# Kernel tuning notes

Measured on AMD Instinct MI355X. Metric: run time of the kernel, lower is better.

Reference implementation:

```python
import jax, jax.numpy as jnp
import numpy as np

N = 100000   # nodes
E = 1600000  # edges
F = 128      # in = hidden channels
L = 4        # num GCN layers
G = 512      # graphs in batch
OUT = 10     # classes
EPS = 1e-5


def setup_inputs() -> dict:
    key = jax.random.key(0)
    ks = jax.random.split(key, 12)
    x = jax.random.normal(ks[0], (N, F), dtype=jnp.float32)
    edge_index = jax.random.randint(ks[1], (2, E), 0, N, dtype=jnp.int64)
    batch = jnp.sort(jax.random.randint(ks[2], (N,), 0, G, dtype=jnp.int64))
    s = 1.0 / np.sqrt(F)
    Ws = jax.random.uniform(ks[3], (L, F, F), jnp.float32, -s, s)
    bs = jax.random.uniform(ks[4], (L, F), jnp.float32, -s, s)
    gammas = jnp.ones((L, F), jnp.float32)
    betas = jnp.zeros((L, F), jnp.float32)
    s1 = 1.0 / np.sqrt(F * L)
    W1 = jax.random.uniform(ks[5], (F * L, F), jnp.float32, -s1, s1)
    b1 = jax.random.uniform(ks[6], (F,), jnp.float32, -s1, s1)
    g1 = jnp.ones((F,), jnp.float32)
    bt1 = jnp.zeros((F,), jnp.float32)
    s2 = 1.0 / np.sqrt(F)
    W2 = jax.random.uniform(ks[7], (F, OUT), jnp.float32, -s2, s2)
    b2 = jax.random.uniform(ks[8], (OUT,), jnp.float32, -s2, s2)
    return {"x": x, "edge_index": edge_index, "batch": batch, "Ws": Ws, "bs": bs,
            "gammas": gammas, "betas": betas, "W1": W1, "b1": b1, "g1": g1,
            "bt1": bt1, "W2": W2, "b2": b2}


def _batch_norm(x, g, b):
    # training-mode BatchNorm1d over the node dim (biased variance)
    mu = jnp.mean(x, axis=0)
    var = jnp.var(x, axis=0)
    return (x - mu) * jax.lax.rsqrt(var + EPS) * g + b


def reference(x, edge_index, batch, Ws, bs, gammas, betas, W1, b1, g1, bt1, W2, b2):
    row, col = edge_index[0], edge_index[1]
    # GCN normalization (add_self_loops=False since normalize=True)
    deg = jax.ops.segment_sum(jnp.ones((E,), x.dtype), col, num_segments=N)
    dinv = jnp.where(deg > 0, jax.lax.rsqrt(deg), 0.0)
    norm = dinv[row] * dinv[col]  # [E]
    pooled = []
    h = x
    for t in range(L):
        hw = h @ Ws[t]                                    # [N, F]
        msg = norm[:, None] * hw[row]                     # gather  [E, F]
        h = jax.ops.segment_sum(msg, col, num_segments=N) + bs[t]  # scatter [N, F]
        h = jax.nn.relu(h)
        h = _batch_norm(h, gammas[t], betas[t])
        pooled.append(jax.ops.segment_sum(h, batch, num_segments=G))  # [G, F]
    z = jnp.concatenate(pooled, axis=1)                   # [G, L*F]
    z = z @ W1 + b1
    z = _batch_norm(z, g1, bt1)
    z = jax.nn.relu(z)
    return z @ W2 + b2                                    # [G, OUT]
```

## Files before the change

kernel.cpp:

```cpp
#include <hip/hip_runtime.h>

#define NN 100000
#define EE 1600000
#define FF 128
#define LL 4
#define GG 512
#define OUTC 10
#define EPSF 1e-5f
#define NSCB ((NN + 255) / 256)

typedef __attribute__((ext_vector_type(8))) short short8;
typedef __attribute__((ext_vector_type(4))) float f32x4;

__device__ inline unsigned bf16rne(float f) {
  unsigned u = __float_as_uint(f);
  return (u + 0x7fffu + ((u >> 16) & 1u)) >> 16;
}
__device__ inline unsigned packbf(float lo, float hi) {
  return bf16rne(lo) | (bf16rne(hi) << 16);
}
__device__ inline float bflo(unsigned u) { return __uint_as_float(u << 16); }
__device__ inline float bfhi(unsigned u) { return __uint_as_float(u & 0xffff0000u); }


__global__ __launch_bounds__(256) void k_deg(const int* __restrict__ col, int* __restrict__ deg) {
  int e = blockIdx.x * 256 + threadIdx.x;
  if (e < EE) atomicAdd(&deg[col[e]], 1);
}

__global__ __launch_bounds__(256) void k_dinv(const int* __restrict__ deg, float* __restrict__ dinv) {
  int n = blockIdx.x * 256 + threadIdx.x;
  if (n < NN) {
    int d = deg[n];
    dinv[n] = d > 0 ? rsqrtf((float)d) : 0.0f;
  }
}

__global__ __launch_bounds__(256) void k_bsum(const int* __restrict__ deg, int* __restrict__ bsum) {
  int i = blockIdx.x * 256 + threadIdx.x;
  int v = (i < NN) ? deg[i] : 0;
#pragma unroll
  for (int off = 32; off > 0; off >>= 1) v += __shfl_down(v, off, 64);
  __shared__ int ws[4];
  if ((threadIdx.x & 63) == 0) ws[threadIdx.x >> 6] = v;
  __syncthreads();
  if (threadIdx.x == 0) bsum[blockIdx.x] = ws[0] + ws[1] + ws[2] + ws[3];
}

__global__ __launch_bounds__(256) void k_rowptr(const int* __restrict__ deg,
                                                const int* __restrict__ bsum,
                                                int* __restrict__ rowptr) {
  __shared__ int sb[512];
  __shared__ int sd[256];
  const int t = threadIdx.x;
  sb[t]       = (t < NSCB) ? bsum[t] : 0;
  sb[t + 256] = (t + 256 < NSCB) ? bsum[t + 256] : 0;
  __syncthreads();
#pragma unroll
  for (int off = 1; off < 512; off <<= 1) {
    int v0 = (t >= off) ? sb[t - off] : 0;
    int v1 = sb[t + 256 - off];
    __syncthreads();
    sb[t] += v0;
    sb[t + 256] += v1;
    __syncthreads();
  }
  const int bpre = (blockIdx.x == 0) ? 0 : sb[blockIdx.x - 1];
  const int i = blockIdx.x * 256 + t;
  const int d = (i < NN) ? deg[i] : 0;
  sd[t] = d;
  __syncthreads();
#pragma unroll
  for (int off = 1; off < 256; off <<= 1) {
    int v = (t >= off) ? sd[t - off] : 0;
    __syncthreads();
    sd[t] += v;
    __syncthreads();
  }
  if (i < NN) rowptr[i] = bpre + sd[t] - d;
  if (blockIdx.x == 0 && t == 0) rowptr[NN] = EE;
}

__global__ __launch_bounds__(256) void k_fill(const int* __restrict__ ei,
                                              const int* __restrict__ rowptr,
                                              int* __restrict__ cnt,
                                              const float* __restrict__ dinv,
                                              int2* __restrict__ ecw) {
  int e = blockIdx.x * 256 + threadIdx.x;
  if (e >= EE) return;
  int r = ei[e];
  int cl = ei[EE + e];
  int slot = rowptr[cl] + atomicAdd(&cnt[cl], 1);
  ecw[slot] = make_int2(r, __float_as_int(dinv[r] * dinv[cl]));
}

__global__ __launch_bounds__(256) void k_bounds(const int* __restrict__ batch, int* __restrict__ gstart) {
  int n = blockIdx.x * 256 + threadIdx.x;
  if (n >= NN) return;
  int b = batch[n];
  if (n == 0) {
    for (int g = 0; g <= b; ++g) gstart[g] = 0;
  } else {
    int bp = batch[n - 1];
    for (int g = bp + 1; g <= b; ++g) gstart[g] = n;
  }
  if (n == NN - 1) {
    for (int g = b + 1; g <= GG; ++g) gstart[g] = NN;
  }
}


__global__ __launch_bounds__(256) void k_cvt(const float* __restrict__ x, unsigned* __restrict__ Ab) {
  int i = blockIdx.x * 256 + threadIdx.x;
  if (i < NN * 64) {
    float2 v = *(const float2*)(x + (size_t)i * 2);
    Ab[i] = packbf(v.x, v.y);
  }
}

__global__ __launch_bounds__(256) void k_wcvt(const float* __restrict__ Ws, uint4* __restrict__ Wf) {
  int tid = blockIdx.x * 256 + threadIdx.x;
  int t = tid >> 12;
  int r = tid & 4095;
  int lane = r & 63;
  int which = (r >> 6) & 1;
  int ct = (r >> 7) & 7;
  int kc = r >> 10;
  int n = ct * 16 + (lane & 15);
  int k0 = kc * 32 + (lane >> 4) * 8;
  const float* W = Ws + t * 16384;
  unsigned h[8];
#pragma unroll
  for (int j = 0; j < 8; ++j) {
    float w = W[(k0 + j) * 128 + n];
    unsigned hb = bf16rne(w);
    if (which == 0) {
      h[j] = hb;
    } else {
      float hf = __uint_as_float(hb << 16);
      h[j] = bf16rne(w - hf);
    }
  }
  uint4 o;
  o.x = h[0] | (h[1] << 16);
  o.y = h[2] | (h[3] << 16);
  o.z = h[4] | (h[5] << 16);
  o.w = h[6] | (h[7] << 16);
  Wf[tid] = o;
}

__global__ __launch_bounds__(256) void k_mm(const unsigned* __restrict__ Ab,
                                            const uint4* __restrict__ Wf,
                                            unsigned* __restrict__ Bb) {
  const int lane = threadIdx.x & 63;
  const int w = threadIdx.x >> 6;
  const int quad = lane >> 4;
  const int m = lane & 15;
  const int rowbase = blockIdx.x * 64 + w * 16;
  const int arow = min(rowbase + m, NN - 1);
  const uint4* A4 = (const uint4*)Ab;
  f32x4 acc[8];
#pragma unroll
  for (int ct = 0; ct < 8; ++ct) acc[ct] = (f32x4){0.f, 0.f, 0.f, 0.f};
#pragma unroll
  for (int kc = 0; kc < 4; ++kc) {
    uint4 av = A4[arow * 16 + kc * 4 + quad];
    short8 af = *(short8*)&av;
#pragma unroll
    for (int ct = 0; ct < 8; ++ct) {
      uint4 bh = Wf[((kc * 8 + ct) * 2 + 0) * 64 + lane];
      uint4 bl = Wf[((kc * 8 + ct) * 2 + 1) * 64 + lane];
      acc[ct] = __builtin_amdgcn_mfma_f32_16x16x32_bf16(af, *(short8*)&bh, acc[ct], 0, 0, 0);
      acc[ct] = __builtin_amdgcn_mfma_f32_16x16x32_bf16(af, *(short8*)&bl, acc[ct], 0, 0, 0);
    }
  }
#pragma unroll
  for (int ct = 0; ct < 8; ++ct) {
#pragma unroll
    for (int r = 0; r < 4; ++r) {
      float v = acc[ct][r];
      float vo = __shfl_xor(v, 1);
      int row = rowbase + quad * 4 + r;
      if ((lane & 1) == 0 && row < NN) {
        Bb[row * 64 + ct * 8 + (m >> 1)] = packbf(v, vo);
      }
    }
  }
}

__global__ __launch_bounds__(256) void k_agg(const unsigned* __restrict__ Bb,
                                             const int* __restrict__ rowptr,
                                             const int2* __restrict__ ecw,
                                             const float* __restrict__ bias,
                                             unsigned* __restrict__ Ar,
                                             float* __restrict__ bnbuf) {
  const int lane = threadIdx.x & 63;
  const int wave = threadIdx.x >> 6;
  const int c = lane * 2;
  const int gwave = blockIdx.x * 4 + wave;
  const int nwaves = gridDim.x * 4;
  const float2 bv = *(const float2*)(bias + c);
  float s0 = 0.f, s1 = 0.f, q0 = 0.f, q1 = 0.f;
  for (int n = gwave; n < NN; n += nwaves) {
    const int beg = rowptr[n];
    const int end = rowptr[n + 1];
    float ax[8], ay[8];
#pragma unroll
    for (int j = 0; j < 8; ++j) { ax[j] = 0.f; ay[j] = 0.f; }
    int2 stage = (beg + lane < end) ? ecw[beg + lane] : make_int2(0, 0);
    for (int base = beg; base < end; base += 64) {
      const int2 cur = stage;
      const int nb = base + 64;
      if (nb < end) {
        const int j = nb + lane;
        stage = (j < end) ? ecw[j] : make_int2(0, 0);
      }
#pragma unroll
      for (int g = 0; g < 4; ++g) {
        if (base + g * 16 < end) {
          int is[16]; float wv[16]; unsigned us[16];
#pragma unroll
          for (int j = 0; j < 16; ++j) {
            is[j] = __shfl(cur.x, g * 16 + j);
            wv[j] = __shfl(__int_as_float(cur.y), g * 16 + j);
          }
#pragma unroll
          for (int j = 0; j < 16; ++j) us[j] = Bb[((unsigned)is[j] << 6) + (unsigned)lane];
#pragma unroll
          for (int j = 0; j < 16; ++j) {
            ax[j & 7] = fmaf(wv[j], bflo(us[j]), ax[j & 7]);
            ay[j & 7] = fmaf(wv[j], bfhi(us[j]), ay[j & 7]);
          }
        }
      }
    }
    float rx = ((ax[0] + ax[1]) + (ax[2] + ax[3])) + ((ax[4] + ax[5]) + (ax[6] + ax[7]));
    float ry = ((ay[0] + ay[1]) + (ay[2] + ay[3])) + ((ay[4] + ay[5]) + (ay[6] + ay[7]));
    rx = fmaxf(rx + bv.x, 0.f);
    ry = fmaxf(ry + bv.y, 0.f);
    Ar[(size_t)n * 64 + lane] = packbf(rx, ry);
    s0 += rx; s1 += ry;
    q0 = fmaf(rx, rx, q0); q1 = fmaf(ry, ry, q1);
  }
  __shared__ float sred[4][256];
  sred[wave][c] = s0;
  sred[wave][c + 1] = s1;
  sred[wave][128 + c] = q0;
  sred[wave][128 + c + 1] = q1;
  __syncthreads();
  const int t = threadIdx.x;
  float tot = sred[0][t] + sred[1][t] + sred[2][t] + sred[3][t];
  atomicAdd(&bnbuf[t], tot);
}

__global__ __launch_bounds__(128) void k_bnfin(const float* __restrict__ bnbuf,
                                               const float* __restrict__ gamma,
                                               const float* __restrict__ beta,
                                               float* __restrict__ bnsc) {
  const int c = threadIdx.x;
  float mu = bnbuf[c] * (1.0f / NN);
  float var = bnbuf[128 + c] * (1.0f / NN) - mu * mu;
  float inv = rsqrtf(var + EPSF);
  float sc = gamma[c] * inv;
  bnsc[c] = sc;
  bnsc[128 + c] = beta[c] - mu * sc;
}

__global__ __launch_bounds__(128) void k_bnapply(const unsigned* __restrict__ Ar,
                                                 const float* __restrict__ bnsc,
                                                 const int* __restrict__ gstart,
                                                 float* __restrict__ pooledt,
                                                 unsigned* __restrict__ Ab) {
  const int g = blockIdx.x >> 3;
  const int sub = blockIdx.x & 7;
  const int s = gstart[g];
  const int e = gstart[g + 1];
  const int cnt = e - s;
  if (cnt <= 0) return;
  const int per = (cnt + 7) >> 3;
  const int ns = s + sub * per;
  const int ne = min(ns + per, e);
  if (ns >= ne) return;
  const int cp = threadIdx.x & 63;
  const int half = threadIdx.x >> 6;
  const float2 sc = *(const float2*)(bnsc + 2 * cp);
  const float2 sh = *(const float2*)(bnsc + 128 + 2 * cp);
  float accx = 0.f, accy = 0.f;
  for (int n = ns + half; n < ne; n += 2) {
    unsigned u = Ar[(size_t)n * 64 + cp];
    float vx = fmaf(bflo(u), sc.x, sh.x);
    float vy = fmaf(bfhi(u), sc.y, sh.y);
    Ab[(size_t)n * 64 + cp] = packbf(vx, vy);
    accx += vx;
    accy += vy;
  }
  atomicAdd(&pooledt[(size_t)g * 512 + 2 * cp], accx);
  atomicAdd(&pooledt[(size_t)g * 512 + 2 * cp + 1], accy);
}


__global__ __launch_bounds__(128) void k_z1(const float* __restrict__ pooled,
                                            const float* __restrict__ W1,
                                            const float* __restrict__ b1,
                                            float* __restrict__ z1) {
  __shared__ float sp[512];
  const int g = blockIdx.x;
  for (int i = threadIdx.x; i < 512; i += 128) sp[i] = pooled[(size_t)g * 512 + i];
  __syncthreads();
  const int c = threadIdx.x;
  float acc = b1[c];
  for (int j = 0; j < 512; ++j) acc = fmaf(sp[j], W1[j * 128 + c], acc);
  z1[(size_t)g * 128 + c] = acc;
}

__global__ __launch_bounds__(128) void k_zstat(const float* __restrict__ z1,
                                               const float* __restrict__ g1,
                                               const float* __restrict__ bt1,
                                               float* __restrict__ zsc) {
  const int c = threadIdx.x;
  float s = 0.f, q = 0.f;
  for (int g = 0; g < GG; ++g) {
    float v = z1[g * 128 + c];
    s += v;
    q = fmaf(v, v, q);
  }
  float mu = s * (1.0f / GG);
  float var = q * (1.0f / GG) - mu * mu;
  float inv = rsqrtf(var + EPSF);
  float sc = g1[c] * inv;
  zsc[c] = sc;
  zsc[128 + c] = bt1[c] - mu * sc;
}

__global__ __launch_bounds__(128) void k_out(const float* __restrict__ z1,
                                             const float* __restrict__ zsc,
                                             const float* __restrict__ W2,
                                             const float* __restrict__ b2,
                                             float* __restrict__ out) {
  __shared__ float zr[128];
  const int g = blockIdx.x;
  const int c = threadIdx.x;
  zr[c] = fmaxf(fmaf(z1[(size_t)g * 128 + c], zsc[c], zsc[128 + c]), 0.f);
  __syncthreads();
  if (c < OUTC) {
    float acc = b2[c];
    for (int k = 0; k < 128; ++k) acc = fmaf(zr[k], W2[k * OUTC + c], acc);
    out[(size_t)g * OUTC + c] = acc;
  }
}


extern "C" void kernel_launch(void* const* d_in, const int* in_sizes, int n_in,
                              void* d_out, int out_size, void* d_ws, size_t ws_size,
                              hipStream_t stream) {
  const float* x      = (const float*)d_in[0];
  const int*   ei     = (const int*)d_in[1];
  const int*   batch  = (const int*)d_in[2];
  const float* Ws     = (const float*)d_in[3];
  const float* bs     = (const float*)d_in[4];
  const float* gammas = (const float*)d_in[5];
  const float* betas  = (const float*)d_in[6];
  const float* W1     = (const float*)d_in[7];
  const float* b1     = (const float*)d_in[8];
  const float* g1     = (const float*)d_in[9];
  const float* bt1    = (const float*)d_in[10];
  const float* W2     = (const float*)d_in[11];
  const float* b2     = (const float*)d_in[12];
  float* out = (float*)d_out;

  char* ws = (char*)d_ws;
  size_t off = 0;
  auto alloc = [&](size_t bytes) -> void* {
    void* p = ws + off;
    off = (off + bytes + 255) & ~(size_t)255;
    return p;
  };
  int*   deg    = (int*)alloc((size_t)NN * 4);
  int*   cnt    = (int*)alloc((size_t)NN * 4);
  float* bnbuf  = (float*)alloc((size_t)LL * 256 * 4);
  float* pooled = (float*)alloc((size_t)GG * 512 * 4);
  size_t zero_bytes = off;
  unsigned* Ar     = (unsigned*)alloc((size_t)NN * 64 * 4);
  unsigned* Ab     = (unsigned*)alloc((size_t)NN * 64 * 4);
  unsigned* Bb     = (unsigned*)alloc((size_t)NN * 64 * 4);
  int2*     ecw    = (int2*)alloc((size_t)EE * 8);
  float*    dinv   = (float*)alloc((size_t)NN * 4);
  int*      rowptr = (int*)alloc((size_t)(NN + 1) * 4);
  int*      bsum   = (int*)alloc((size_t)NSCB * 4);
  int*      gstart = (int*)alloc((size_t)(GG + 1) * 4);
  uint4*    Wf     = (uint4*)alloc((size_t)LL * 4096 * 16);
  float*    z1     = (float*)alloc((size_t)GG * FF * 4);
  float*    bnsc   = (float*)alloc(256 * 4);
  float*    zsc    = (float*)alloc(256 * 4);
  (void)ws_size; (void)in_sizes; (void)n_in; (void)out_size;

  hipMemsetAsync(d_ws, 0, zero_bytes, stream);

  k_deg<<<(EE + 255) / 256, 256, 0, stream>>>(ei + EE, deg);
  k_dinv<<<(NN + 255) / 256, 256, 0, stream>>>(deg, dinv);
  k_bsum<<<NSCB, 256, 0, stream>>>(deg, bsum);
  k_rowptr<<<NSCB, 256, 0, stream>>>(deg, bsum, rowptr);
  k_fill<<<(EE + 255) / 256, 256, 0, stream>>>(ei, rowptr, cnt, dinv, ecw);
  k_bounds<<<(NN + 255) / 256, 256, 0, stream>>>(batch, gstart);
  k_cvt<<<(NN * 64 + 255) / 256, 256, 0, stream>>>(x, Ab);
  k_wcvt<<<64, 256, 0, stream>>>(Ws, Wf);

  for (int t = 0; t < LL; ++t) {
    k_mm<<<(NN + 63) / 64, 256, 0, stream>>>(Ab, Wf + (size_t)t * 4096, Bb);
    k_agg<<<2048, 256, 0, stream>>>(Bb, rowptr, ecw, bs + t * FF, Ar, bnbuf + t * 256);
    k_bnfin<<<1, 128, 0, stream>>>(bnbuf + t * 256, gammas + t * FF, betas + t * FF, bnsc);
    k_bnapply<<<GG * 8, 128, 0, stream>>>(Ar, bnsc, gstart, pooled + t * FF, Ab);
  }

  k_z1<<<GG, 128, 0, stream>>>(pooled, W1, b1, z1);
  k_zstat<<<1, 128, 0, stream>>>(z1, g1, bt1, zsc);
  k_out<<<GG, 128, 0, stream>>>(z1, zsc, W2, b2, out);
}
```

Before: 858.2 us.

## Split wave into half-waves gathering 8-byte rows with double-buffered prefetch

The aggregation kernel now has each half-wave handle a different edge, with each lane loading 8 bytes (4 bf16 channels) per neighbor row instead of 4 bytes. Gathers for the next group of 8 edges are issued before the current group's FMAs, using two register buffers. The two halves are combined with a cross-lane shuffle, and launch bounds now request 8 blocks per CU for more occupancy. The intent is wider gather loads and more memory-level parallelism. The cost is fewer independent accumulators, extra shuffles, and dropping the previous prefetch of the edge list.

```diff
diff --git a/kernel.cpp b/kernel.cpp
--- a/kernel.cpp
+++ b/kernel.cpp
@@ -188,68 +188,84 @@
   }
 }
 
-__global__ __launch_bounds__(256) void k_agg(const unsigned* __restrict__ Bb,
-                                             const int* __restrict__ rowptr,
-                                             const int2* __restrict__ ecw,
-                                             const float* __restrict__ bias,
-                                             unsigned* __restrict__ Ar,
-                                             float* __restrict__ bnbuf) {
+__global__ __launch_bounds__(256, 8) void k_agg(const unsigned* __restrict__ Bb,
+                                                const int* __restrict__ rowptr,
+                                                const int2* __restrict__ ecw,
+                                                const float* __restrict__ bias,
+                                                unsigned* __restrict__ Ar,
+                                                float* __restrict__ bnbuf) {
   const int lane = threadIdx.x & 63;
   const int wave = threadIdx.x >> 6;
-  const int c = lane * 2;
+  const int h = lane >> 5;
+  const int cl = lane & 31;
   const int gwave = blockIdx.x * 4 + wave;
   const int nwaves = gridDim.x * 4;
-  const float2 bv = *(const float2*)(bias + c);
-  float s0 = 0.f, s1 = 0.f, q0 = 0.f, q1 = 0.f;
+  const uint2* B2 = (const uint2*)Bb;
+  const float4 bv = *(const float4*)(bias + 4 * cl);
+  float s0 = 0.f, s1 = 0.f, s2 = 0.f, s3 = 0.f;
+  float q0 = 0.f, q1 = 0.f, q2 = 0.f, q3 = 0.f;
   for (int n = gwave; n < NN; n += nwaves) {
     const int beg = rowptr[n];
     const int end = rowptr[n + 1];
-    float ax[8], ay[8];
-#pragma unroll
-    for (int j = 0; j < 8; ++j) { ax[j] = 0.f; ay[j] = 0.f; }
-    int2 stage = (beg + lane < end) ? ecw[beg + lane] : make_int2(0, 0);
+    float a0 = 0.f, a1 = 0.f, a2 = 0.f, a3 = 0.f;
     for (int base = beg; base < end; base += 64) {
-      const int2 cur = stage;
-      const int nb = base + 64;
-      if (nb < end) {
-        const int j = nb + lane;
-        stage = (j < end) ? ecw[j] : make_int2(0, 0);
+      const int myj = base + lane;
+      const int2 cur = (myj < end) ? ecw[myj] : make_int2(0, 0);
+      uint2 u0[4], u1[4];
+#pragma unroll
+      for (int j = 0; j < 4; ++j) {
+        int src = __shfl(cur.x, 2 * j + h);
+        u0[j] = B2[(unsigned)src * 32 + (unsigned)cl];
       }
 #pragma unroll
-      for (int g = 0; g < 4; ++g) {
-        if (base + g * 16 < end) {
-          int is[16]; float wv[16]; unsigned us[16];
-#pragma unroll
-          for (int j = 0; j < 16; ++j) {
-            is[j] = __shfl(cur.x, g * 16 + j);
-            wv[j] = __shfl(__int_as_float(cur.y), g * 16 + j);
+      for (int g = 0; g < 8; ++g) {
+        if (base + (g + 1) * 8 < end) {
+#pragma unroll
+          for (int j = 0; j < 4; ++j) {
+            int src = __shfl(cur.x, 2 * ((g + 1) * 4 + j) + h);
+            if (g & 1) u0[j] = B2[(unsigned)src * 32 + (unsigned)cl];
+            else       u1[j] = B2[(unsigned)src * 32 + (unsigned)cl];
           }
-#pragma unroll
-          for (int j = 0; j < 16; ++j) us[j] = Bb[((unsigned)is[j] << 6) + (unsigned)lane];
-#pragma unroll
-          for (int j = 0; j < 16; ++j) {
-            ax[j & 7] = fmaf(wv[j], bflo(us[j]), ax[j & 7]);
-            ay[j & 7] = fmaf(wv[j], bfhi(us[j]), ay[j & 7]);
+        }
+        if (base + g * 8 < end) {
+#pragma unroll
+          for (int j = 0; j < 4; ++j) {
+            float w = __shfl(__int_as_float(cur.y), 2 * (g * 4 + j) + h);
+            uint2 u = (g & 1) ? u1[j] : u0[j];
+            a0 = fmaf(w, bflo(u.x), a0);
+            a1 = fmaf(w, bfhi(u.x), a1);
+            a2 = fmaf(w, bflo(u.y), a2);
+            a3 = fmaf(w, bfhi(u.y), a3);
           }
         }
       }
     }
-    float rx = ((ax[0] + ax[1]) + (ax[2] + ax[3])) + ((ax[4] + ax[5]) + (ax[6] + ax[7]));
-    float ry = ((ay[0] + ay[1]) + (ay[2] + ay[3])) + ((ay[4] + ay[5]) + (ay[6] + ay[7]));
-    rx = fmaxf(rx + bv.x, 0.f);
-    ry = fmaxf(ry + bv.y, 0.f);
-    Ar[(size_t)n * 64 + lane] = packbf(rx, ry);
-    s0 += rx; s1 += ry;
-    q0 = fmaf(rx, rx, q0); q1 = fmaf(ry, ry, q1);
+    a0 += __shfl_xor(a0, 32);
+    a1 += __shfl_xor(a1, 32);
+    a2 += __shfl_xor(a2, 32);
+    a3 += __shfl_xor(a3, 32);
+    a0 = fmaxf(a0 + bv.x, 0.f);
+    a1 = fmaxf(a1 + bv.y, 0.f);
+    a2 = fmaxf(a2 + bv.z, 0.f);
+    a3 = fmaxf(a3 + bv.w, 0.f);
+    if (h == 0) {
+      uint2 o;
+      o.x = packbf(a0, a1);
+      o.y = packbf(a2, a3);
+      ((uint2*)Ar)[(size_t)n * 32 + cl] = o;
+      s0 += a0; s1 += a1; s2 += a2; s3 += a3;
+      q0 = fmaf(a0, a0, q0); q1 = fmaf(a1, a1, q1);
+      q2 = fmaf(a2, a2, q2); q3 = fmaf(a3, a3, q3);
+    }
   }
   __shared__ float sred[4][256];
-  sred[wave][c] = s0;
-  sred[wave][c + 1] = s1;
-  sred[wave][128 + c] = q0;
-  sred[wave][128 + c + 1] = q1;
+  if (h == 0) {
+    *(float4*)&sred[wave][4 * cl] = make_float4(s0, s1, s2, s3);
+    *(float4*)&sred[wave][128 + 4 * cl] = make_float4(q0, q1, q2, q3);
+  }
   __syncthreads();
   const int t = threadIdx.x;
-  float tot = sred[0][t] + sred[1][t] + sred[2][t] + sred[3][t];
+  float tot = (sred[0][t] + sred[1][t]) + (sred[2][t] + sred[3][t]);
   atomicAdd(&bnbuf[t], tot);
 }
 
```

Measured after the change: 1.031 ms. 1.2x slower.

## Fold BatchNorm apply into next matmul and pool raw activations in aggregation

Applied to the files above, without the earlier changes.

Removes the per-layer bn-apply pass. The batch-norm affine is now applied on the fly in the next layer's matmul input load, and graph pooling is done on raw activations inside the aggregation kernel with per-node atomics. Pooled sums are then corrected with scale*sum + shift*count in a tiny kernel. This saves a full read and write of the node-feature matrix per layer, but adds 128 global atomics per node into a 512x128 buffer, which may contend because nodes are sorted by graph. It also changes rounding slightly, since the raw activations are bf16 and the affine is applied before repacking.

```diff
diff --git a/kernel.cpp b/kernel.cpp
--- a/kernel.cpp
+++ b/kernel.cpp
@@ -116,6 +116,11 @@
     float2 v = *(const float2*)(x + (size_t)i * 2);
     Ab[i] = packbf(v.x, v.y);
   }
+}
+
+__global__ __launch_bounds__(128) void k_id(float* __restrict__ idt) {
+  idt[threadIdx.x] = 1.0f;
+  idt[128 + threadIdx.x] = 0.0f;
 }
 
 __global__ __launch_bounds__(256) void k_wcvt(const float* __restrict__ Ws, uint4* __restrict__ Wf) {
@@ -149,7 +154,8 @@
   Wf[tid] = o;
 }
 
-__global__ __launch_bounds__(256) void k_mm(const unsigned* __restrict__ Ab,
+__global__ __launch_bounds__(256) void k_mm(const unsigned* __restrict__ Hb,
+                                            const float* __restrict__ aff,
                                             const uint4* __restrict__ Wf,
                                             unsigned* __restrict__ Bb) {
   const int lane = threadIdx.x & 63;
@@ -158,14 +164,24 @@
   const int m = lane & 15;
   const int rowbase = blockIdx.x * 64 + w * 16;
   const int arow = min(rowbase + m, NN - 1);
-  const uint4* A4 = (const uint4*)Ab;
+  const uint4* A4 = (const uint4*)Hb;
   f32x4 acc[8];
 #pragma unroll
   for (int ct = 0; ct < 8; ++ct) acc[ct] = (f32x4){0.f, 0.f, 0.f, 0.f};
 #pragma unroll
   for (int kc = 0; kc < 4; ++kc) {
     uint4 av = A4[arow * 16 + kc * 4 + quad];
-    short8 af = *(short8*)&av;
+    const int cb = kc * 32 + quad * 8;
+    float4 sc0 = *(const float4*)(aff + cb);
+    float4 sc1 = *(const float4*)(aff + cb + 4);
+    float4 sh0 = *(const float4*)(aff + 128 + cb);
+    float4 sh1 = *(const float4*)(aff + 128 + cb + 4);
+    uint4 hv;
+    hv.x = packbf(fmaf(bflo(av.x), sc0.x, sh0.x), fmaf(bfhi(av.x), sc0.y, sh0.y));
+    hv.y = packbf(fmaf(bflo(av.y), sc0.z, sh0.z), fmaf(bfhi(av.y), sc0.w, sh0.w));
+    hv.z = packbf(fmaf(bflo(av.z), sc1.x, sh1.x), fmaf(bfhi(av.z), sc1.y, sh1.y));
+    hv.w = packbf(fmaf(bflo(av.w), sc1.z, sh1.z), fmaf(bfhi(av.w), sc1.w, sh1.w));
+    short8 af = *(short8*)&hv;
 #pragma unroll
     for (int ct = 0; ct < 8; ++ct) {
       uint4 bh = Wf[((kc * 8 + ct) * 2 + 0) * 64 + lane];
@@ -192,8 +208,10 @@
                                              const int* __restrict__ rowptr,
                                              const int2* __restrict__ ecw,
                                              const float* __restrict__ bias,
+                                             const int* __restrict__ batch,
                                              unsigned* __restrict__ Ar,
-                                             float* __restrict__ bnbuf) {
+                                             float* __restrict__ bnbuf,
+                                             float* __restrict__ praw) {
   const int lane = threadIdx.x & 63;
   const int wave = threadIdx.x >> 6;
   const int c = lane * 2;
@@ -241,6 +259,9 @@
     Ar[(size_t)n * 64 + lane] = packbf(rx, ry);
     s0 += rx; s1 += ry;
     q0 = fmaf(rx, rx, q0); q1 = fmaf(ry, ry, q1);
+    const int bg = batch[n];
+    atomicAdd(&praw[(size_t)bg * 128 + c], rx);
+    atomicAdd(&praw[(size_t)bg * 128 + c + 1], ry);
   }
   __shared__ float sred[4][256];
   sred[wave][c] = s0;
@@ -249,7 +270,7 @@
   sred[wave][128 + c + 1] = q1;
   __syncthreads();
   const int t = threadIdx.x;
-  float tot = sred[0][t] + sred[1][t] + sred[2][t] + sred[3][t];
+  float tot = (sred[0][t] + sred[1][t]) + (sred[2][t] + sred[3][t]);
   atomicAdd(&bnbuf[t], tot);
 }
 
@@ -266,36 +287,14 @@
   bnsc[128 + c] = beta[c] - mu * sc;
 }
 
-__global__ __launch_bounds__(128) void k_bnapply(const unsigned* __restrict__ Ar,
-                                                 const float* __restrict__ bnsc,
-                                                 const int* __restrict__ gstart,
-                                                 float* __restrict__ pooledt,
-                                                 unsigned* __restrict__ Ab) {
-  const int g = blockIdx.x >> 3;
-  const int sub = blockIdx.x & 7;
-  const int s = gstart[g];
-  const int e = gstart[g + 1];
-  const int cnt = e - s;
-  if (cnt <= 0) return;
-  const int per = (cnt + 7) >> 3;
-  const int ns = s + sub * per;
-  const int ne = min(ns + per, e);
-  if (ns >= ne) return;
-  const int cp = threadIdx.x & 63;
-  const int half = threadIdx.x >> 6;
-  const float2 sc = *(const float2*)(bnsc + 2 * cp);
-  const float2 sh = *(const float2*)(bnsc + 128 + 2 * cp);
-  float accx = 0.f, accy = 0.f;
-  for (int n = ns + half; n < ne; n += 2) {
-    unsigned u = Ar[(size_t)n * 64 + cp];
-    float vx = fmaf(bflo(u), sc.x, sh.x);
-    float vy = fmaf(bfhi(u), sc.y, sh.y);
-    Ab[(size_t)n * 64 + cp] = packbf(vx, vy);
-    accx += vx;
-    accy += vy;
-  }
-  atomicAdd(&pooledt[(size_t)g * 512 + 2 * cp], accx);
-  atomicAdd(&pooledt[(size_t)g * 512 + 2 * cp + 1], accy);
+__global__ __launch_bounds__(128) void k_pool(const float* __restrict__ praw,
+                                              const float* __restrict__ bnsc,
+                                              const int* __restrict__ gstart,
+                                              float* __restrict__ pooledt) {
+  const int g = blockIdx.x;
+  const int c = threadIdx.x;
+  const float cntf = (float)(gstart[g + 1] - gstart[g]);
+  pooledt[(size_t)g * 512 + c] = fmaf(bnsc[c], praw[(size_t)g * 128 + c], bnsc[128 + c] * cntf);
 }
 
 
@@ -378,10 +377,11 @@
   int*   deg    = (int*)alloc((size_t)NN * 4);
   int*   cnt    = (int*)alloc((size_t)NN * 4);
   float* bnbuf  = (float*)alloc((size_t)LL * 256 * 4);
-  float* pooled = (float*)alloc((size_t)GG * 512 * 4);
+  float* praw   = (float*)alloc((size_t)LL * GG * 128 * 4);
   size_t zero_bytes = off;
+  float* pooled    = (float*)alloc((size_t)GG * 512 * 4);
   unsigned* Ar     = (unsigned*)alloc((size_t)NN * 64 * 4);
-  unsigned* Ab     = (unsigned*)alloc((size_t)NN * 64 * 4);
+  unsigned* Ab0    = (unsigned*)alloc((size_t)NN * 64 * 4);
   unsigned* Bb     = (unsigned*)alloc((size_t)NN * 64 * 4);
   int2*     ecw    = (int2*)alloc((size_t)EE * 8);
   float*    dinv   = (float*)alloc((size_t)NN * 4);
@@ -390,7 +390,8 @@
   int*      gstart = (int*)alloc((size_t)(GG + 1) * 4);
   uint4*    Wf     = (uint4*)alloc((size_t)LL * 4096 * 16);
   float*    z1     = (float*)alloc((size_t)GG * FF * 4);
-  float*    bnsc   = (float*)alloc(256 * 4);
+  float*    bnsc   = (float*)alloc((size_t)LL * 256 * 4);
+  float*    idt    = (float*)alloc(256 * 4);
   float*    zsc    = (float*)alloc(256 * 4);
   (void)ws_size; (void)in_sizes; (void)n_in; (void)out_size;
 
@@ -402,14 +403,20 @@
   k_rowptr<<<NSCB, 256, 0, stream>>>(deg, bsum, rowptr);
   k_fill<<<(EE + 255) / 256, 256, 0, stream>>>(ei, rowptr, cnt, dinv, ecw);
   k_bounds<<<(NN + 255) / 256, 256, 0, stream>>>(batch, gstart);
-  k_cvt<<<(NN * 64 + 255) / 256, 256, 0, stream>>>(x, Ab);
+  k_cvt<<<(NN * 64 + 255) / 256, 256, 0, stream>>>(x, Ab0);
+  k_id<<<1, 128, 0, stream>>>(idt);
   k_wcvt<<<64, 256, 0, stream>>>(Ws, Wf);
 
   for (int t = 0; t < LL; ++t) {
-    k_mm<<<(NN + 63) / 64, 256, 0, stream>>>(Ab, Wf + (size_t)t * 4096, Bb);
-    k_agg<<<2048, 256, 0, stream>>>(Bb, rowptr, ecw, bs + t * FF, Ar, bnbuf + t * 256);
-    k_bnfin<<<1, 128, 0, stream>>>(bnbuf + t * 256, gammas + t * FF, betas + t * FF, bnsc);
-    k_bnapply<<<GG * 8, 128, 0, stream>>>(Ar, bnsc, gstart, pooled + t * FF, Ab);
+    const unsigned* Hb = (t == 0) ? Ab0 : Ar;
+    const float* aff = (t == 0) ? idt : (bnsc + (size_t)(t - 1) * 256);
+    k_mm<<<(NN + 63) / 64, 256, 0, stream>>>(Hb, aff, Wf + (size_t)t * 4096, Bb);
+    k_agg<<<2048, 256, 0, stream>>>(Bb, rowptr, ecw, bs + t * FF, batch, Ar,
+                                    bnbuf + t * 256, praw + (size_t)t * GG * 128);
+    k_bnfin<<<1, 128, 0, stream>>>(bnbuf + t * 256, gammas + t * FF, betas + t * FF,
+                                   bnsc + (size_t)t * 256);
+    k_pool<<<GG, 128, 0, stream>>>(praw + (size_t)t * GG * 128, bnsc + (size_t)t * 256,
+                                   gstart, pooled + t * FF);
   }
 
   k_z1<<<GG, 128, 0, stream>>>(pooled, W1, b1, z1);
```

Measured after the change: 1.184 ms. 1.38x slower.
